# Kernel optimization log

Hardware: AMD Instinct MI355X
Metric: run time of the kernel (lower is better)

The kernel has to match this reference:

```python
import jax, jax.numpy as jnp
import numpy as np

NUM_FEATURES = 256
GROUP_SIZE = 4
NUM_GROUPS = NUM_FEATURES // GROUP_SIZE
EPS = 1e-3


def setup_inputs() -> dict:
    key = jax.random.key(0)
    x = jax.random.normal(key, (64, NUM_FEATURES, 56, 56), dtype=jnp.float32)
    return {"x": x}


def reference(x):
    # Group ZCA whitening (training-mode path of _Whitening.forward).
    b, c, w, h = x.shape
    G, gs = NUM_GROUPS, GROUP_SIZE
    n = b * w * h
    # per-channel mean, grouped: [G, gs, 1]
    m = x.mean(axis=0).reshape(c, -1).mean(axis=-1).reshape(G, gs, 1)
    # [G, gs, b*w*h], mean-centered
    T = x.transpose(1, 0, 2, 3).reshape(G, gs, n) - m
    # unnormalized covariance (matches torch.bmm(T, T^T) in source)
    f_cov = jnp.einsum('gik,gjk->gij', T, T)
    eye = jnp.eye(gs, dtype=x.dtype)
    f_cov_shrinked = (1.0 - EPS) * f_cov + EPS * eye  # [G, gs, gs]
    u, s, _ = jnp.linalg.svd(f_cov_shrinked)
    sqrt_s = jnp.sqrt(s + EPS)[:, :, None]  # [G, gs, 1]
    # pca = u^T T / sqrt(s); zca = u pca
    pca = jnp.einsum('gji,gjk->gik', u, T) / sqrt_s
    zca = jnp.einsum('gij,gjk->gik', u, pca)
    decorrelated = zca.reshape(c, b, w, h).transpose(1, 0, 2, 3)
    return decorrelated
```

## Files before the change

### kernel.cpp

```cpp
#include <hip/hip_runtime.h>
#include <math.h>

#define BATCH   64
#define NFEAT   256
#define GS      4
#define NG      64
#define WH      3136
#define PLANEQ  784
#define NTOT    (BATCH*WH)
#define EPSV    1e-3

typedef float vf4 __attribute__((ext_vector_type(4)));

__global__ __launch_bounds__(256) void wh_reduce(const float* __restrict__ x,
                                                 float* __restrict__ partials) {
    const int blk = blockIdx.x;
    const int b = blk >> 6;
    const int g = blk & 63;
    const vf4* __restrict__ xin =
        (const vf4*)(x + (size_t)b * ((size_t)NFEAT * WH) + (size_t)g * (GS * WH));

    float s0=0.f,s1=0.f,s2=0.f,s3=0.f;
    float p0=0.f,p1=0.f,p2=0.f,p3=0.f,p4=0.f,p5=0.f,p6=0.f,p7=0.f,p8=0.f,p9=0.f;

    for (int q = threadIdx.x; q < PLANEQ; q += 256) {
        vf4 v0 = xin[q];
        vf4 v1 = xin[q + PLANEQ];
        vf4 v2 = xin[q + 2*PLANEQ];
        vf4 v3 = xin[q + 3*PLANEQ];
        #pragma unroll
        for (int k = 0; k < 4; ++k) {
            float a = v0[k], bb = v1[k], c = v2[k], d = v3[k];
            s0 += a; s1 += bb; s2 += c; s3 += d;
            p0 = fmaf(a,  a,  p0);
            p1 = fmaf(a,  bb, p1);
            p2 = fmaf(a,  c,  p2);
            p3 = fmaf(a,  d,  p3);
            p4 = fmaf(bb, bb, p4);
            p5 = fmaf(bb, c,  p5);
            p6 = fmaf(bb, d,  p6);
            p7 = fmaf(c,  c,  p7);
            p8 = fmaf(c,  d,  p8);
            p9 = fmaf(d,  d,  p9);
        }
    }

    float vals[14] = {s0,s1,s2,s3,p0,p1,p2,p3,p4,p5,p6,p7,p8,p9};
    #pragma unroll
    for (int q = 0; q < 14; ++q) {
        float v = vals[q];
        #pragma unroll
        for (int off = 32; off > 0; off >>= 1) v += __shfl_down(v, off, 64);
        vals[q] = v;
    }

    __shared__ float lds[4][14];
    const int wave = threadIdx.x >> 6;
    const int lane = threadIdx.x & 63;
    if (lane == 0) {
        #pragma unroll
        for (int q = 0; q < 14; ++q) lds[wave][q] = vals[q];
    }
    __syncthreads();
    if (threadIdx.x < 14) {
        float v = lds[0][threadIdx.x] + lds[1][threadIdx.x]
                + lds[2][threadIdx.x] + lds[3][threadIdx.x];
        partials[((size_t)(g * BATCH + b)) * 14 + threadIdx.x] = v;
    }
}

__global__ __launch_bounds__(64) void wh_eigen(const float* __restrict__ partials,
                                               float* __restrict__ wm) {
    const int g = blockIdx.x;
    const int b = threadIdx.x;

    const float* base = partials + ((size_t)(g * BATCH + b)) * 14;
    double acc[14];
    #pragma unroll
    for (int q = 0; q < 14; ++q) acc[q] = (double)base[q];

    #pragma unroll
    for (int off = 32; off > 0; off >>= 1) {
        #pragma unroll
        for (int q = 0; q < 14; ++q) acc[q] += __shfl_xor(acc[q], off, 64);
    }

    if (b != 0) return;

    const double n = (double)NTOT;
    double m[4];
    #pragma unroll
    for (int i = 0; i < 4; ++i) m[i] = acc[i] / n;

    const int pi[10] = {0,0,0,0,1,1,1,2,2,3};
    const int pj[10] = {0,1,2,3,1,2,3,2,3,3};

    double A[4][4];
    #pragma unroll
    for (int t = 0; t < 10; ++t) {
        double cov = acc[4 + t] - n * m[pi[t]] * m[pj[t]];
        double v = (1.0 - EPSV) * cov + ((pi[t] == pj[t]) ? EPSV : 0.0);
        A[pi[t]][pj[t]] = v;
        A[pj[t]][pi[t]] = v;
    }

    double V[4][4] = {{1,0,0,0},{0,1,0,0},{0,0,1,0},{0,0,0,1}};

    const double tr = A[0][0] + A[1][1] + A[2][2] + A[3][3];
    const double tol = 1e-26 * tr * tr + 1e-300;

    const int rp[6] = {0,0,0,1,1,2};
    const int rq[6] = {1,2,3,2,3,3};

    for (int sweep = 0; sweep < 10; ++sweep) {
        double off = 0.0;
        #pragma unroll
        for (int t = 0; t < 6; ++t) off += A[rp[t]][rq[t]] * A[rp[t]][rq[t]];
        if (off < tol) break;

        #pragma unroll
        for (int t = 0; t < 6; ++t) {
            const int p = rp[t], q = rq[t];
            double apq = A[p][q];
            if (apq * apq < 1e-60) continue;
            double theta = (A[q][q] - A[p][p]) / (2.0 * apq);
            double tt = ((theta >= 0.0) ? 1.0 : -1.0) /
                        (fabs(theta) + sqrt(theta * theta + 1.0));
            double c = 1.0 / sqrt(tt * tt + 1.0);
            double s = tt * c;
            #pragma unroll
            for (int k = 0; k < 4; ++k) {
                double akp = A[k][p], akq = A[k][q];
                A[k][p] = c * akp - s * akq;
                A[k][q] = s * akp + c * akq;
            }
            #pragma unroll
            for (int k = 0; k < 4; ++k) {
                double apk = A[p][k], aqk = A[q][k];
                A[p][k] = c * apk - s * aqk;
                A[q][k] = s * apk + c * aqk;
            }
            #pragma unroll
            for (int k = 0; k < 4; ++k) {
                double vkp = V[k][p], vkq = V[k][q];
                V[k][p] = c * vkp - s * vkq;
                V[k][q] = s * vkp + c * vkq;
            }
        }
    }

    double isq[4];
    #pragma unroll
    for (int k = 0; k < 4; ++k) isq[k] = 1.0 / sqrt(A[k][k] + EPSV);

    float* wo = wm + g * 20;
    #pragma unroll
    for (int i = 0; i < 4; ++i) {
        #pragma unroll
        for (int j = 0; j < 4; ++j) {
            double w = 0.0;
            #pragma unroll
            for (int k = 0; k < 4; ++k) w += V[i][k] * V[j][k] * isq[k];
            wo[i * 4 + j] = (float)w;
        }
    }
    #pragma unroll
    for (int i = 0; i < 4; ++i) wo[16 + i] = (float)m[i];
}

__global__ __launch_bounds__(256) void wh_apply(const float* __restrict__ x,
                                                const float* __restrict__ wm,
                                                float* __restrict__ out) {
    const int blk = blockIdx.x;
    const int b = blk >> 6;
    const int g = blk & 63;

    __shared__ float sW[20];
    if (threadIdx.x < 20) sW[threadIdx.x] = wm[g * 20 + threadIdx.x];
    __syncthreads();

    float W[4][4], mm[4];
    #pragma unroll
    for (int i = 0; i < 4; ++i) {
        #pragma unroll
        for (int j = 0; j < 4; ++j) W[i][j] = sW[i * 4 + j];
        mm[i] = sW[16 + i];
    }

    const size_t off = (size_t)b * ((size_t)NFEAT * WH) + (size_t)g * (GS * WH);
    const vf4* __restrict__ xin = (const vf4*)(x + off);
    vf4* __restrict__ o = (vf4*)(out + off);

    for (int q = threadIdx.x; q < PLANEQ; q += 256) {
        vf4 v[4];
        v[0] = xin[q];
        v[1] = xin[q + PLANEQ];
        v[2] = xin[q + 2 * PLANEQ];
        v[3] = xin[q + 3 * PLANEQ];

        float c[4][4];
        #pragma unroll
        for (int j = 0; j < 4; ++j) {
            #pragma unroll
            for (int k = 0; k < 4; ++k) c[j][k] = v[j][k] - mm[j];
        }

        #pragma unroll
        for (int i = 0; i < 4; ++i) {
            vf4 r;
            #pragma unroll
            for (int k = 0; k < 4; ++k) {
                r[k] = fmaf(W[i][0], c[0][k],
                       fmaf(W[i][1], c[1][k],
                       fmaf(W[i][2], c[2][k], W[i][3] * c[3][k])));
            }
            __builtin_nontemporal_store(r, &o[q + i * PLANEQ]);
        }
    }
}

extern "C" void kernel_launch(void* const* d_in, const int* in_sizes, int n_in,
                              void* d_out, int out_size, void* d_ws, size_t ws_size,
                              hipStream_t stream) {
    const float* x = (const float*)d_in[0];
    float* out = (float*)d_out;

    float* partials = (float*)d_ws;
    float* wm       = partials + (size_t)NG * BATCH * 14;

    wh_reduce<<<BATCH * NG, 256, 0, stream>>>(x, partials);
    wh_eigen<<<NG, 64, 0, stream>>>(partials, wm);
    wh_apply<<<BATCH * NG, 256, 0, stream>>>(x, wm, out);
}
```

Measured before the change: 110.2 us.

## Fuse eigen solve into reduction via last-block atomic counter; fold mean into bias

```diff
diff --git a/kernel.cpp b/kernel.cpp
--- a/kernel.cpp
+++ b/kernel.cpp
@@ -9,41 +9,54 @@
 #define PLANEQ  784
 #define NTOT    (BATCH*WH)
 #define EPSV    1e-3
+#define PREC    16
 
 typedef float vf4 __attribute__((ext_vector_type(4)));
 
-__global__ __launch_bounds__(256) void wh_reduce(const float* __restrict__ x,
-                                                 float* __restrict__ partials) {
+__global__ __launch_bounds__(256) void wh_reduce_eigen(const float* __restrict__ x,
+                                                       float* __restrict__ partials,
+                                                       float* __restrict__ wm,
+                                                       int* __restrict__ cnt) {
     const int blk = blockIdx.x;
     const int b = blk >> 6;
     const int g = blk & 63;
+    const int tid = threadIdx.x;
     const vf4* __restrict__ xin =
         (const vf4*)(x + (size_t)b * ((size_t)NFEAT * WH) + (size_t)g * (GS * WH));
 
+    vf4 a0 = xin[tid];             vf4 a1 = xin[tid + 256];             vf4 a2 = xin[tid + 512];
+    vf4 b0 = xin[PLANEQ + tid];    vf4 b1 = xin[PLANEQ + tid + 256];    vf4 b2 = xin[PLANEQ + tid + 512];
+    vf4 c0 = xin[2*PLANEQ + tid];  vf4 c1 = xin[2*PLANEQ + tid + 256];  vf4 c2 = xin[2*PLANEQ + tid + 512];
+    vf4 d0 = xin[3*PLANEQ + tid];  vf4 d1 = xin[3*PLANEQ + tid + 256];  vf4 d2 = xin[3*PLANEQ + tid + 512];
+
     float s0=0.f,s1=0.f,s2=0.f,s3=0.f;
     float p0=0.f,p1=0.f,p2=0.f,p3=0.f,p4=0.f,p5=0.f,p6=0.f,p7=0.f,p8=0.f,p9=0.f;
 
-    for (int q = threadIdx.x; q < PLANEQ; q += 256) {
-        vf4 v0 = xin[q];
-        vf4 v1 = xin[q + PLANEQ];
-        vf4 v2 = xin[q + 2*PLANEQ];
-        vf4 v3 = xin[q + 3*PLANEQ];
-        #pragma unroll
-        for (int k = 0; k < 4; ++k) {
-            float a = v0[k], bb = v1[k], c = v2[k], d = v3[k];
-            s0 += a; s1 += bb; s2 += c; s3 += d;
-            p0 = fmaf(a,  a,  p0);
-            p1 = fmaf(a,  bb, p1);
-            p2 = fmaf(a,  c,  p2);
-            p3 = fmaf(a,  d,  p3);
-            p4 = fmaf(bb, bb, p4);
-            p5 = fmaf(bb, c,  p5);
-            p6 = fmaf(bb, d,  p6);
-            p7 = fmaf(c,  c,  p7);
-            p8 = fmaf(c,  d,  p8);
-            p9 = fmaf(d,  d,  p9);
-        }
-    }
+#define ACC4(va, vb, vc, vd)                                         \
+    {                                                                \
+        _Pragma("unroll")                                            \
+        for (int k = 0; k < 4; ++k) {                                \
+            float A = (va)[k], B = (vb)[k], C = (vc)[k], D = (vd)[k];\
+            s0 += A; s1 += B; s2 += C; s3 += D;                      \
+            p0 = fmaf(A, A, p0);  p1 = fmaf(A, B, p1);               \
+            p2 = fmaf(A, C, p2);  p3 = fmaf(A, D, p3);               \
+            p4 = fmaf(B, B, p4);  p5 = fmaf(B, C, p5);               \
+            p6 = fmaf(B, D, p6);  p7 = fmaf(C, C, p7);               \
+            p8 = fmaf(C, D, p8);  p9 = fmaf(D, D, p9);               \
+        }                                                            \
+    }
+
+    ACC4(a0, b0, c0, d0);
+    ACC4(a1, b1, c1, d1);
+    ACC4(a2, b2, c2, d2);
+    if (tid < PLANEQ - 768) {
+        vf4 at = xin[768 + tid];
+        vf4 bt = xin[PLANEQ + 768 + tid];
+        vf4 ct = xin[2*PLANEQ + 768 + tid];
+        vf4 dt = xin[3*PLANEQ + 768 + tid];
+        ACC4(at, bt, ct, dt);
+    }
+#undef ACC4
 
     float vals[14] = {s0,s1,s2,s3,p0,p1,p2,p3,p4,p5,p6,p7,p8,p9};
     #pragma unroll
@@ -55,26 +68,30 @@
     }
 
     __shared__ float lds[4][14];
-    const int wave = threadIdx.x >> 6;
-    const int lane = threadIdx.x & 63;
+    __shared__ int isLast;
+    const int wave = tid >> 6;
+    const int lane = tid & 63;
     if (lane == 0) {
         #pragma unroll
         for (int q = 0; q < 14; ++q) lds[wave][q] = vals[q];
     }
     __syncthreads();
-    if (threadIdx.x < 14) {
-        float v = lds[0][threadIdx.x] + lds[1][threadIdx.x]
-                + lds[2][threadIdx.x] + lds[3][threadIdx.x];
-        partials[((size_t)(g * BATCH + b)) * 14 + threadIdx.x] = v;
-    }
-}
-
-__global__ __launch_bounds__(64) void wh_eigen(const float* __restrict__ partials,
-                                               float* __restrict__ wm) {
-    const int g = blockIdx.x;
-    const int b = threadIdx.x;
-
-    const float* base = partials + ((size_t)(g * BATCH + b)) * 14;
+    if (tid < 14) {
+        float v = lds[0][tid] + lds[1][tid] + lds[2][tid] + lds[3][tid];
+        partials[((size_t)(g * BATCH + b)) * PREC + tid] = v;
+    }
+    __threadfence();
+    __syncthreads();
+    if (tid == 0) {
+        int prev = atomicAdd(&cnt[g], 1);
+        isLast = (prev == BATCH - 1);
+    }
+    __syncthreads();
+    if (!isLast || tid >= 64) return;
+
+    __threadfence();
+
+    const float* base = partials + ((size_t)(g * BATCH + tid)) * PREC;
     double acc[14];
     #pragma unroll
     for (int q = 0; q < 14; ++q) acc[q] = (double)base[q];
@@ -85,7 +102,7 @@
         for (int q = 0; q < 14; ++q) acc[q] += __shfl_xor(acc[q], off, 64);
     }
 
-    if (b != 0) return;
+    if (tid != 0) return;
 
     const double n = (double)NTOT;
     double m[4];
@@ -153,7 +170,8 @@
     #pragma unroll
     for (int k = 0; k < 4; ++k) isq[k] = 1.0 / sqrt(A[k][k] + EPSV);
 
-    float* wo = wm + g * 20;
+    float* wo = wm + g * 24;
+    double Wd[4][4];
     #pragma unroll
     for (int i = 0; i < 4; ++i) {
         #pragma unroll
@@ -161,11 +179,16 @@
             double w = 0.0;
             #pragma unroll
             for (int k = 0; k < 4; ++k) w += V[i][k] * V[j][k] * isq[k];
+            Wd[i][j] = w;
             wo[i * 4 + j] = (float)w;
         }
     }
     #pragma unroll
-    for (int i = 0; i < 4; ++i) wo[16 + i] = (float)m[i];
+    for (int i = 0; i < 4; ++i) {
+        double wmI = Wd[i][0]*m[0] + Wd[i][1]*m[1] + Wd[i][2]*m[2] + Wd[i][3]*m[3];
+        wo[16 + i] = (float)(-wmI);
+        wo[20 + i] = (float)m[i];
+    }
 }
 
 __global__ __launch_bounds__(256) void wh_apply(const float* __restrict__ x,
@@ -174,49 +197,49 @@
     const int blk = blockIdx.x;
     const int b = blk >> 6;
     const int g = blk & 63;
+    const int tid = threadIdx.x;
 
     __shared__ float sW[20];
-    if (threadIdx.x < 20) sW[threadIdx.x] = wm[g * 20 + threadIdx.x];
-    __syncthreads();
-
-    float W[4][4], mm[4];
+    if (tid < 20) sW[tid] = wm[g * 24 + tid];
+    __syncthreads();
+
+    float W[4][4], nwm[4];
     #pragma unroll
     for (int i = 0; i < 4; ++i) {
         #pragma unroll
         for (int j = 0; j < 4; ++j) W[i][j] = sW[i * 4 + j];
-        mm[i] = sW[16 + i];
+        nwm[i] = sW[16 + i];
     }
 
     const size_t off = (size_t)b * ((size_t)NFEAT * WH) + (size_t)g * (GS * WH);
     const vf4* __restrict__ xin = (const vf4*)(x + off);
     vf4* __restrict__ o = (vf4*)(out + off);
 
-    for (int q = threadIdx.x; q < PLANEQ; q += 256) {
-        vf4 v[4];
-        v[0] = xin[q];
-        v[1] = xin[q + PLANEQ];
-        v[2] = xin[q + 2 * PLANEQ];
-        v[3] = xin[q + 3 * PLANEQ];
-
-        float c[4][4];
-        #pragma unroll
-        for (int j = 0; j < 4; ++j) {
-            #pragma unroll
-            for (int k = 0; k < 4; ++k) c[j][k] = v[j][k] - mm[j];
-        }
-
-        #pragma unroll
-        for (int i = 0; i < 4; ++i) {
-            vf4 r;
-            #pragma unroll
-            for (int k = 0; k < 4; ++k) {
-                r[k] = fmaf(W[i][0], c[0][k],
-                       fmaf(W[i][1], c[1][k],
-                       fmaf(W[i][2], c[2][k], W[i][3] * c[3][k])));
-            }
-            __builtin_nontemporal_store(r, &o[q + i * PLANEQ]);
-        }
-    }
+#define APPLY4(q)                                                              \
+    {                                                                          \
+        vf4 v0 = xin[(q)];                                                     \
+        vf4 v1 = xin[(q) + PLANEQ];                                            \
+        vf4 v2 = xin[(q) + 2 * PLANEQ];                                        \
+        vf4 v3 = xin[(q) + 3 * PLANEQ];                                        \
+        _Pragma("unroll")                                                      \
+        for (int i = 0; i < 4; ++i) {                                          \
+            vf4 r;                                                             \
+            _Pragma("unroll")                                                  \
+            for (int k = 0; k < 4; ++k) {                                      \
+                r[k] = fmaf(W[i][0], v0[k],                                    \
+                       fmaf(W[i][1], v1[k],                                    \
+                       fmaf(W[i][2], v2[k],                                    \
+                       fmaf(W[i][3], v3[k], nwm[i]))));                        \
+            }                                                                  \
+            __builtin_nontemporal_store(r, &o[(q) + i * PLANEQ]);              \
+        }                                                                      \
+    }
+
+    APPLY4(tid);
+    APPLY4(tid + 256);
+    APPLY4(tid + 512);
+    if (tid < PLANEQ - 768) APPLY4(tid + 768);
+#undef APPLY4
 }
 
 extern "C" void kernel_launch(void* const* d_in, const int* in_sizes, int n_in,
@@ -226,9 +249,10 @@
     float* out = (float*)d_out;
 
     float* partials = (float*)d_ws;
-    float* wm       = partials + (size_t)NG * BATCH * 14;
-
-    wh_reduce<<<BATCH * NG, 256, 0, stream>>>(x, partials);
-    wh_eigen<<<NG, 64, 0, stream>>>(partials, wm);
+    float* wm       = partials + (size_t)NG * BATCH * PREC;
+    int*   cnt      = (int*)(wm + NG * 24);
+
+    hipMemsetAsync(cnt, 0, NG * sizeof(int), stream);
+    wh_reduce_eigen<<<BATCH * NG, 256, 0, stream>>>(x, partials, wm, cnt);
     wh_apply<<<BATCH * NG, 256, 0, stream>>>(x, wm, out);
 }
```

Measured after the change: 394.9 us. 258% more time.

## Fuse reduce, eigen-solve and apply into one cooperative kernel holding data in registers

Applied to the files above, without the earlier changes.

```diff
diff --git a/kernel.cpp b/kernel.cpp
--- a/kernel.cpp
+++ b/kernel.cpp
@@ -1,5 +1,8 @@
 #include <hip/hip_runtime.h>
+#include <hip/hip_cooperative_groups.h>
 #include <math.h>
+
+namespace cg = cooperative_groups;
 
 #define BATCH   64
 #define NFEAT   256
@@ -9,84 +12,12 @@
 #define PLANEQ  784
 #define NTOT    (BATCH*WH)
 #define EPSV    1e-3
+#define PREC    16
+#define COOP_GRID 2048
 
 typedef float vf4 __attribute__((ext_vector_type(4)));
 
-__global__ __launch_bounds__(256) void wh_reduce(const float* __restrict__ x,
-                                                 float* __restrict__ partials) {
-    const int blk = blockIdx.x;
-    const int b = blk >> 6;
-    const int g = blk & 63;
-    const vf4* __restrict__ xin =
-        (const vf4*)(x + (size_t)b * ((size_t)NFEAT * WH) + (size_t)g * (GS * WH));
-
-    float s0=0.f,s1=0.f,s2=0.f,s3=0.f;
-    float p0=0.f,p1=0.f,p2=0.f,p3=0.f,p4=0.f,p5=0.f,p6=0.f,p7=0.f,p8=0.f,p9=0.f;
-
-    for (int q = threadIdx.x; q < PLANEQ; q += 256) {
-        vf4 v0 = xin[q];
-        vf4 v1 = xin[q + PLANEQ];
-        vf4 v2 = xin[q + 2*PLANEQ];
-        vf4 v3 = xin[q + 3*PLANEQ];
-        #pragma unroll
-        for (int k = 0; k < 4; ++k) {
-            float a = v0[k], bb = v1[k], c = v2[k], d = v3[k];
-            s0 += a; s1 += bb; s2 += c; s3 += d;
-            p0 = fmaf(a,  a,  p0);
-            p1 = fmaf(a,  bb, p1);
-            p2 = fmaf(a,  c,  p2);
-            p3 = fmaf(a,  d,  p3);
-            p4 = fmaf(bb, bb, p4);
-            p5 = fmaf(bb, c,  p5);
-            p6 = fmaf(bb, d,  p6);
-            p7 = fmaf(c,  c,  p7);
-            p8 = fmaf(c,  d,  p8);
-            p9 = fmaf(d,  d,  p9);
-        }
-    }
-
-    float vals[14] = {s0,s1,s2,s3,p0,p1,p2,p3,p4,p5,p6,p7,p8,p9};
-    #pragma unroll
-    for (int q = 0; q < 14; ++q) {
-        float v = vals[q];
-        #pragma unroll
-        for (int off = 32; off > 0; off >>= 1) v += __shfl_down(v, off, 64);
-        vals[q] = v;
-    }
-
-    __shared__ float lds[4][14];
-    const int wave = threadIdx.x >> 6;
-    const int lane = threadIdx.x & 63;
-    if (lane == 0) {
-        #pragma unroll
-        for (int q = 0; q < 14; ++q) lds[wave][q] = vals[q];
-    }
-    __syncthreads();
-    if (threadIdx.x < 14) {
-        float v = lds[0][threadIdx.x] + lds[1][threadIdx.x]
-                + lds[2][threadIdx.x] + lds[3][threadIdx.x];
-        partials[((size_t)(g * BATCH + b)) * 14 + threadIdx.x] = v;
-    }
-}
-
-__global__ __launch_bounds__(64) void wh_eigen(const float* __restrict__ partials,
-                                               float* __restrict__ wm) {
-    const int g = blockIdx.x;
-    const int b = threadIdx.x;
-
-    const float* base = partials + ((size_t)(g * BATCH + b)) * 14;
-    double acc[14];
-    #pragma unroll
-    for (int q = 0; q < 14; ++q) acc[q] = (double)base[q];
-
-    #pragma unroll
-    for (int off = 32; off > 0; off >>= 1) {
-        #pragma unroll
-        for (int q = 0; q < 14; ++q) acc[q] += __shfl_xor(acc[q], off, 64);
-    }
-
-    if (b != 0) return;
-
+__device__ void solve_group(const double* acc, float* wo) {
     const double n = (double)NTOT;
     double m[4];
     #pragma unroll
@@ -105,10 +36,8 @@
     }
 
     double V[4][4] = {{1,0,0,0},{0,1,0,0},{0,0,1,0},{0,0,0,1}};
-
     const double tr = A[0][0] + A[1][1] + A[2][2] + A[3][3];
     const double tol = 1e-26 * tr * tr + 1e-300;
-
     const int rp[6] = {0,0,0,1,1,2};
     const int rq[6] = {1,2,3,2,3,3};
 
@@ -117,7 +46,6 @@
         #pragma unroll
         for (int t = 0; t < 6; ++t) off += A[rp[t]][rq[t]] * A[rp[t]][rq[t]];
         if (off < tol) break;
-
         #pragma unroll
         for (int t = 0; t < 6; ++t) {
             const int p = rp[t], q = rq[t];
@@ -153,7 +81,7 @@
     #pragma unroll
     for (int k = 0; k < 4; ++k) isq[k] = 1.0 / sqrt(A[k][k] + EPSV);
 
-    float* wo = wm + g * 20;
+    double Wd[4][4];
     #pragma unroll
     for (int i = 0; i < 4; ++i) {
         #pragma unroll
@@ -161,11 +89,241 @@
             double w = 0.0;
             #pragma unroll
             for (int k = 0; k < 4; ++k) w += V[i][k] * V[j][k] * isq[k];
+            Wd[i][j] = w;
             wo[i * 4 + j] = (float)w;
         }
     }
     #pragma unroll
-    for (int i = 0; i < 4; ++i) wo[16 + i] = (float)m[i];
+    for (int i = 0; i < 4; ++i) {
+        double wmI = Wd[i][0]*m[0] + Wd[i][1]*m[1] + Wd[i][2]*m[2] + Wd[i][3]*m[3];
+        wo[16 + i] = (float)(-wmI);
+        wo[20 + i] = (float)m[i];
+    }
+}
+
+__global__ __launch_bounds__(256, 8) void wh_fused(const float* __restrict__ x,
+                                                   float* __restrict__ partials,
+                                                   float* __restrict__ wm,
+                                                   float* __restrict__ out) {
+    cg::grid_group grid = cg::this_grid();
+    const int B   = blockIdx.x;
+    const int tid = threadIdx.x;
+    const int b   = B >> 5;
+    const int g0  = (B & 31) << 1;
+
+    const size_t base0 = (size_t)b * ((size_t)NFEAT * WH) + (size_t)g0 * (GS * WH);
+    const vf4* __restrict__ x0 = (const vf4*)(x + base0);
+    const vf4* __restrict__ x1 = x0 + GS * PLANEQ;
+
+    const bool tail = (tid < PLANEQ - 3 * 256);
+    const int  qt   = 768 + (tid & 15);
+
+    vf4 d0[16], d1[16];
+    #pragma unroll
+    for (int c = 0; c < 4; ++c) {
+        #pragma unroll
+        for (int r = 0; r < 3; ++r) {
+            d0[c*4+r] = x0[c*PLANEQ + tid + 256*r];
+            d1[c*4+r] = x1[c*PLANEQ + tid + 256*r];
+        }
+    }
+    #pragma unroll
+    for (int c = 0; c < 4; ++c) {
+        vf4 t0 = x0[c*PLANEQ + qt];
+        vf4 t1 = x1[c*PLANEQ + qt];
+        if (!tail) { t0 = (vf4){0.f,0.f,0.f,0.f}; t1 = (vf4){0.f,0.f,0.f,0.f}; }
+        d0[c*4+3] = t0;
+        d1[c*4+3] = t1;
+    }
+
+    float vv[28];
+    #pragma unroll
+    for (int q = 0; q < 28; ++q) vv[q] = 0.f;
+
+#define REDUCE_TILE(D, OFF)                                              \
+    {                                                                    \
+        _Pragma("unroll")                                                \
+        for (int r = 0; r < 4; ++r) {                                    \
+            _Pragma("unroll")                                            \
+            for (int k = 0; k < 4; ++k) {                                \
+                float A = D[0*4+r][k], Bv = D[1*4+r][k];                 \
+                float C = D[2*4+r][k], Dv = D[3*4+r][k];                 \
+                vv[OFF+0] += A; vv[OFF+1] += Bv;                         \
+                vv[OFF+2] += C; vv[OFF+3] += Dv;                         \
+                vv[OFF+4]  = fmaf(A,  A,  vv[OFF+4]);                    \
+                vv[OFF+5]  = fmaf(A,  Bv, vv[OFF+5]);                    \
+                vv[OFF+6]  = fmaf(A,  C,  vv[OFF+6]);                    \
+                vv[OFF+7]  = fmaf(A,  Dv, vv[OFF+7]);                    \
+                vv[OFF+8]  = fmaf(Bv, Bv, vv[OFF+8]);                    \
+                vv[OFF+9]  = fmaf(Bv, C,  vv[OFF+9]);                    \
+                vv[OFF+10] = fmaf(Bv, Dv, vv[OFF+10]);                   \
+                vv[OFF+11] = fmaf(C,  C,  vv[OFF+11]);                   \
+                vv[OFF+12] = fmaf(C,  Dv, vv[OFF+12]);                   \
+                vv[OFF+13] = fmaf(Dv, Dv, vv[OFF+13]);                   \
+            }                                                            \
+        }                                                                \
+    }
+    REDUCE_TILE(d0, 0);
+    REDUCE_TILE(d1, 14);
+#undef REDUCE_TILE
+
+    #pragma unroll
+    for (int q = 0; q < 28; ++q) {
+        float v = vv[q];
+        #pragma unroll
+        for (int off = 32; off > 0; off >>= 1) v += __shfl_down(v, off, 64);
+        vv[q] = v;
+    }
+
+    __shared__ float lds[4][28];
+    const int wave = tid >> 6;
+    const int lane = tid & 63;
+    if (lane == 0) {
+        #pragma unroll
+        for (int q = 0; q < 28; ++q) lds[wave][q] = vv[q];
+    }
+    __syncthreads();
+    if (tid < 28) {
+        float v = lds[0][tid] + lds[1][tid] + lds[2][tid] + lds[3][tid];
+        const int s = tid / 14, q = tid - s * 14;
+        partials[((size_t)((g0 + s) * BATCH + b)) * PREC + q] = v;
+    }
+
+    grid.sync();
+
+    if (B < NG && tid < 64) {
+        const float* bse = partials + ((size_t)(B * BATCH + tid)) * PREC;
+        double acc[14];
+        #pragma unroll
+        for (int q = 0; q < 14; ++q) acc[q] = (double)bse[q];
+        #pragma unroll
+        for (int off = 32; off > 0; off >>= 1) {
+            #pragma unroll
+            for (int q = 0; q < 14; ++q) acc[q] += __shfl_xor(acc[q], off, 64);
+        }
+        if (tid == 0) solve_group(acc, wm + B * 24);
+    }
+
+    grid.sync();
+
+    __shared__ float sW[40];
+    if (tid < 20)                      sW[tid]        = wm[g0 * 24 + tid];
+    else if (tid >= 32 && tid < 52)    sW[tid - 12]   = wm[(g0 + 1) * 24 + (tid - 32)];
+    __syncthreads();
+
+    float W0[4][4], n0[4], W1[4][4], n1[4];
+    #pragma unroll
+    for (int i = 0; i < 4; ++i) {
+        #pragma unroll
+        for (int j = 0; j < 4; ++j) { W0[i][j] = sW[i*4+j]; W1[i][j] = sW[20+i*4+j]; }
+        n0[i] = sW[16 + i];
+        n1[i] = sW[36 + i];
+    }
+
+    vf4* __restrict__ o0 = (vf4*)(out + base0);
+    vf4* __restrict__ o1 = o0 + GS * PLANEQ;
+
+#define APPLY_TILE(D, W, NW, O)                                          \
+    {                                                                    \
+        _Pragma("unroll")                                                \
+        for (int i = 0; i < 4; ++i) {                                    \
+            _Pragma("unroll")                                            \
+            for (int r = 0; r < 3; ++r) {                                \
+                vf4 rr;                                                  \
+                _Pragma("unroll")                                        \
+                for (int k = 0; k < 4; ++k) {                            \
+                    rr[k] = fmaf(W[i][0], D[0*4+r][k],                   \
+                            fmaf(W[i][1], D[1*4+r][k],                   \
+                            fmaf(W[i][2], D[2*4+r][k],                   \
+                            fmaf(W[i][3], D[3*4+r][k], NW[i]))));        \
+                }                                                        \
+                __builtin_nontemporal_store(rr, &O[i*PLANEQ + tid + 256*r]); \
+            }                                                            \
+            if (tail) {                                                  \
+                vf4 rr;                                                  \
+                _Pragma("unroll")                                        \
+                for (int k = 0; k < 4; ++k) {                            \
+                    rr[k] = fmaf(W[i][0], D[0*4+3][k],                   \
+                            fmaf(W[i][1], D[1*4+3][k],                   \
+                            fmaf(W[i][2], D[2*4+3][k],                   \
+                            fmaf(W[i][3], D[3*4+3][k], NW[i]))));        \
+                }                                                        \
+                __builtin_nontemporal_store(rr, &O[i*PLANEQ + qt]);      \
+            }                                                            \
+        }                                                                \
+    }
+    APPLY_TILE(d0, W0, n0, o0);
+    APPLY_TILE(d1, W1, n1, o1);
+#undef APPLY_TILE
+}
+
+__global__ __launch_bounds__(256) void wh_reduce(const float* __restrict__ x,
+                                                 float* __restrict__ partials) {
+    const int blk = blockIdx.x;
+    const int b = blk >> 6;
+    const int g = blk & 63;
+    const int tid = threadIdx.x;
+    const vf4* __restrict__ xin =
+        (const vf4*)(x + (size_t)b * ((size_t)NFEAT * WH) + (size_t)g * (GS * WH));
+
+    float s0=0.f,s1=0.f,s2=0.f,s3=0.f;
+    float p0=0.f,p1=0.f,p2=0.f,p3=0.f,p4=0.f,p5=0.f,p6=0.f,p7=0.f,p8=0.f,p9=0.f;
+
+    for (int q = tid; q < PLANEQ; q += 256) {
+        vf4 v0 = xin[q];
+        vf4 v1 = xin[q + PLANEQ];
+        vf4 v2 = xin[q + 2*PLANEQ];
+        vf4 v3 = xin[q + 3*PLANEQ];
+        #pragma unroll
+        for (int k = 0; k < 4; ++k) {
+            float A = v0[k], Bv = v1[k], C = v2[k], D = v3[k];
+            s0 += A; s1 += Bv; s2 += C; s3 += D;
+            p0 = fmaf(A, A, p0);   p1 = fmaf(A, Bv, p1);
+            p2 = fmaf(A, C, p2);   p3 = fmaf(A, D, p3);
+            p4 = fmaf(Bv, Bv, p4); p5 = fmaf(Bv, C, p5);
+            p6 = fmaf(Bv, D, p6);  p7 = fmaf(C, C, p7);
+            p8 = fmaf(C, D, p8);   p9 = fmaf(D, D, p9);
+        }
+    }
+
+    float vals[14] = {s0,s1,s2,s3,p0,p1,p2,p3,p4,p5,p6,p7,p8,p9};
+    #pragma unroll
+    for (int q = 0; q < 14; ++q) {
+        float v = vals[q];
+        #pragma unroll
+        for (int off = 32; off > 0; off >>= 1) v += __shfl_down(v, off, 64);
+        vals[q] = v;
+    }
+
+    __shared__ float lds2[4][14];
+    const int wave = tid >> 6;
+    const int lane = tid & 63;
+    if (lane == 0) {
+        #pragma unroll
+        for (int q = 0; q < 14; ++q) lds2[wave][q] = vals[q];
+    }
+    __syncthreads();
+    if (tid < 14) {
+        float v = lds2[0][tid] + lds2[1][tid] + lds2[2][tid] + lds2[3][tid];
+        partials[((size_t)(g * BATCH + b)) * PREC + tid] = v;
+    }
+}
+
+__global__ __launch_bounds__(64) void wh_eigen(const float* __restrict__ partials,
+                                               float* __restrict__ wm) {
+    const int g = blockIdx.x;
+    const int b = threadIdx.x;
+    const float* base = partials + ((size_t)(g * BATCH + b)) * PREC;
+    double acc[14];
+    #pragma unroll
+    for (int q = 0; q < 14; ++q) acc[q] = (double)base[q];
+    #pragma unroll
+    for (int off = 32; off > 0; off >>= 1) {
+        #pragma unroll
+        for (int q = 0; q < 14; ++q) acc[q] += __shfl_xor(acc[q], off, 64);
+    }
+    if (b != 0) return;
+    solve_group(acc, wm + g * 24);
 }
 
 __global__ __launch_bounds__(256) void wh_apply(const float* __restrict__ x,
@@ -174,45 +332,38 @@
     const int blk = blockIdx.x;
     const int b = blk >> 6;
     const int g = blk & 63;
+    const int tid = threadIdx.x;
 
     __shared__ float sW[20];
-    if (threadIdx.x < 20) sW[threadIdx.x] = wm[g * 20 + threadIdx.x];
+    if (tid < 20) sW[tid] = wm[g * 24 + tid];
     __syncthreads();
 
-    float W[4][4], mm[4];
+    float W[4][4], nwm[4];
     #pragma unroll
     for (int i = 0; i < 4; ++i) {
         #pragma unroll
         for (int j = 0; j < 4; ++j) W[i][j] = sW[i * 4 + j];
-        mm[i] = sW[16 + i];
+        nwm[i] = sW[16 + i];
     }
 
     const size_t off = (size_t)b * ((size_t)NFEAT * WH) + (size_t)g * (GS * WH);
     const vf4* __restrict__ xin = (const vf4*)(x + off);
     vf4* __restrict__ o = (vf4*)(out + off);
 
-    for (int q = threadIdx.x; q < PLANEQ; q += 256) {
-        vf4 v[4];
-        v[0] = xin[q];
-        v[1] = xin[q + PLANEQ];
-        v[2] = xin[q + 2 * PLANEQ];
-        v[3] = xin[q + 3 * PLANEQ];
-
-        float c[4][4];
-        #pragma unroll
-        for (int j = 0; j < 4; ++j) {
-            #pragma unroll
-            for (int k = 0; k < 4; ++k) c[j][k] = v[j][k] - mm[j];
-        }
-
+    for (int q = tid; q < PLANEQ; q += 256) {
+        vf4 v0 = xin[q];
+        vf4 v1 = xin[q + PLANEQ];
+        vf4 v2 = xin[q + 2 * PLANEQ];
+        vf4 v3 = xin[q + 3 * PLANEQ];
         #pragma unroll
         for (int i = 0; i < 4; ++i) {
             vf4 r;
             #pragma unroll
             for (int k = 0; k < 4; ++k) {
-                r[k] = fmaf(W[i][0], c[0][k],
-                       fmaf(W[i][1], c[1][k],
-                       fmaf(W[i][2], c[2][k], W[i][3] * c[3][k])));
+                r[k] = fmaf(W[i][0], v0[k],
+                       fmaf(W[i][1], v1[k],
+                       fmaf(W[i][2], v2[k],
+                       fmaf(W[i][3], v3[k], nwm[i]))));
             }
             __builtin_nontemporal_store(r, &o[q + i * PLANEQ]);
         }
@@ -226,7 +377,20 @@
     float* out = (float*)d_out;
 
     float* partials = (float*)d_ws;
-    float* wm       = partials + (size_t)NG * BATCH * 14;
+    float* wm       = partials + (size_t)NG * BATCH * PREC;
+
+    int maxBlk = 0, numCU = 0;
+    hipOccupancyMaxActiveBlocksPerMultiprocessor(&maxBlk, (const void*)wh_fused, 256, 0);
+    hipDeviceGetAttribute(&numCU, hipDeviceAttributeMultiprocessorCount, 0);
+
+    bool coop_ok = (maxBlk * numCU >= COOP_GRID);
+    if (coop_ok) {
+        void* args[4] = {(void*)&x, (void*)&partials, (void*)&wm, (void*)&out};
+        hipError_t e = hipLaunchCooperativeKernel((const void*)wh_fused,
+                                                  dim3(COOP_GRID), dim3(256),
+                                                  args, 0, stream);
+        if (e == hipSuccess) return;
+    }
 
     wh_reduce<<<BATCH * NG, 256, 0, stream>>>(x, partials);
     wh_eigen<<<NG, 64, 0, stream>>>(partials, wm);
```

New measurement: 111.9 us. No clear change (+1.5%).

## Fuse reduce, eigen-solve and apply into one register-resident pass with inter-block flags

Applied to the files above, without the earlier changes.

```diff
diff --git a/kernel.cpp b/kernel.cpp
--- a/kernel.cpp
+++ b/kernel.cpp
@@ -11,82 +11,22 @@
 #define EPSV    1e-3
 
 typedef float vf4 __attribute__((ext_vector_type(4)));
-
-__global__ __launch_bounds__(256) void wh_reduce(const float* __restrict__ x,
-                                                 float* __restrict__ partials) {
-    const int blk = blockIdx.x;
-    const int b = blk >> 6;
-    const int g = blk & 63;
-    const vf4* __restrict__ xin =
-        (const vf4*)(x + (size_t)b * ((size_t)NFEAT * WH) + (size_t)g * (GS * WH));
-
-    float s0=0.f,s1=0.f,s2=0.f,s3=0.f;
-    float p0=0.f,p1=0.f,p2=0.f,p3=0.f,p4=0.f,p5=0.f,p6=0.f,p7=0.f,p8=0.f,p9=0.f;
-
-    for (int q = threadIdx.x; q < PLANEQ; q += 256) {
-        vf4 v0 = xin[q];
-        vf4 v1 = xin[q + PLANEQ];
-        vf4 v2 = xin[q + 2*PLANEQ];
-        vf4 v3 = xin[q + 3*PLANEQ];
-        #pragma unroll
-        for (int k = 0; k < 4; ++k) {
-            float a = v0[k], bb = v1[k], c = v2[k], d = v3[k];
-            s0 += a; s1 += bb; s2 += c; s3 += d;
-            p0 = fmaf(a,  a,  p0);
-            p1 = fmaf(a,  bb, p1);
-            p2 = fmaf(a,  c,  p2);
-            p3 = fmaf(a,  d,  p3);
-            p4 = fmaf(bb, bb, p4);
-            p5 = fmaf(bb, c,  p5);
-            p6 = fmaf(bb, d,  p6);
-            p7 = fmaf(c,  c,  p7);
-            p8 = fmaf(c,  d,  p8);
-            p9 = fmaf(d,  d,  p9);
-        }
-    }
-
-    float vals[14] = {s0,s1,s2,s3,p0,p1,p2,p3,p4,p5,p6,p7,p8,p9};
-    #pragma unroll
-    for (int q = 0; q < 14; ++q) {
-        float v = vals[q];
-        #pragma unroll
-        for (int off = 32; off > 0; off >>= 1) v += __shfl_down(v, off, 64);
-        vals[q] = v;
-    }
-
-    __shared__ float lds[4][14];
-    const int wave = threadIdx.x >> 6;
-    const int lane = threadIdx.x & 63;
-    if (lane == 0) {
-        #pragma unroll
-        for (int q = 0; q < 14; ++q) lds[wave][q] = vals[q];
-    }
-    __syncthreads();
-    if (threadIdx.x < 14) {
-        float v = lds[0][threadIdx.x] + lds[1][threadIdx.x]
-                + lds[2][threadIdx.x] + lds[3][threadIdx.x];
-        partials[((size_t)(g * BATCH + b)) * 14 + threadIdx.x] = v;
-    }
-}
-
-__global__ __launch_bounds__(64) void wh_eigen(const float* __restrict__ partials,
-                                               float* __restrict__ wm) {
-    const int g = blockIdx.x;
-    const int b = threadIdx.x;
-
-    const float* base = partials + ((size_t)(g * BATCH + b)) * 14;
-    double acc[14];
-    #pragma unroll
-    for (int q = 0; q < 14; ++q) acc[q] = (double)base[q];
-
-    #pragma unroll
-    for (int off = 32; off > 0; off >>= 1) {
-        #pragma unroll
-        for (int q = 0; q < 14; ++q) acc[q] += __shfl_xor(acc[q], off, 64);
-    }
-
-    if (b != 0) return;
-
+typedef unsigned long long u64;
+
+#define AL64(p)    __hip_atomic_load((p), __ATOMIC_RELAXED, __HIP_MEMORY_SCOPE_AGENT)
+#define AX64(p,v)  __hip_atomic_exchange((p), (v), __ATOMIC_RELAXED, __HIP_MEMORY_SCOPE_AGENT)
+#define ALI(p)     __hip_atomic_load((p), __ATOMIC_RELAXED, __HIP_MEMORY_SCOPE_AGENT)
+#define AXI(p,v)   __hip_atomic_exchange((p), (v), __ATOMIC_RELAXED, __HIP_MEMORY_SCOPE_AGENT)
+#define AAI(p,v)   __hip_atomic_fetch_add((p), (v), __ATOMIC_RELAXED, __HIP_MEMORY_SCOPE_AGENT)
+
+__device__ inline u64 pack2(float a, float b) {
+    union { float f[2]; u64 u; } t; t.f[0] = a; t.f[1] = b; return t.u;
+}
+__device__ inline void unpack2(u64 u, float& a, float& b) {
+    union { u64 u; float f[2]; } t; t.u = u; a = t.f[0]; b = t.f[1];
+}
+
+__device__ void solve_group(const double* acc, float* wo) {
     const double n = (double)NTOT;
     double m[4];
     #pragma unroll
@@ -105,10 +45,8 @@
     }
 
     double V[4][4] = {{1,0,0,0},{0,1,0,0},{0,0,1,0},{0,0,0,1}};
-
     const double tr = A[0][0] + A[1][1] + A[2][2] + A[3][3];
     const double tol = 1e-26 * tr * tr + 1e-300;
-
     const int rp[6] = {0,0,0,1,1,2};
     const int rq[6] = {1,2,3,2,3,3};
 
@@ -117,7 +55,6 @@
         #pragma unroll
         for (int t = 0; t < 6; ++t) off += A[rp[t]][rq[t]] * A[rp[t]][rq[t]];
         if (off < tol) break;
-
         #pragma unroll
         for (int t = 0; t < 6; ++t) {
             const int p = rp[t], q = rq[t];
@@ -153,7 +90,7 @@
     #pragma unroll
     for (int k = 0; k < 4; ++k) isq[k] = 1.0 / sqrt(A[k][k] + EPSV);
 
-    float* wo = wm + g * 20;
+    double Wd[4][4];
     #pragma unroll
     for (int i = 0; i < 4; ++i) {
         #pragma unroll
@@ -161,60 +98,172 @@
             double w = 0.0;
             #pragma unroll
             for (int k = 0; k < 4; ++k) w += V[i][k] * V[j][k] * isq[k];
+            Wd[i][j] = w;
             wo[i * 4 + j] = (float)w;
         }
     }
     #pragma unroll
-    for (int i = 0; i < 4; ++i) wo[16 + i] = (float)m[i];
-}
-
-__global__ __launch_bounds__(256) void wh_apply(const float* __restrict__ x,
-                                                const float* __restrict__ wm,
-                                                float* __restrict__ out) {
-    const int blk = blockIdx.x;
-    const int b = blk >> 6;
-    const int g = blk & 63;
-
-    __shared__ float sW[20];
-    if (threadIdx.x < 20) sW[threadIdx.x] = wm[g * 20 + threadIdx.x];
-    __syncthreads();
-
-    float W[4][4], mm[4];
-    #pragma unroll
-    for (int i = 0; i < 4; ++i) {
-        #pragma unroll
-        for (int j = 0; j < 4; ++j) W[i][j] = sW[i * 4 + j];
-        mm[i] = sW[16 + i];
-    }
+    for (int i = 0; i < 4; ++i) {
+        double wmI = Wd[i][0]*m[0] + Wd[i][1]*m[1] + Wd[i][2]*m[2] + Wd[i][3]*m[3];
+        wo[16 + i] = (float)(-wmI);
+    }
+}
+
+__global__ __launch_bounds__(256, 2) void wh_onepass(const float* __restrict__ x,
+                                                     u64* __restrict__ partials,
+                                                     u64* __restrict__ wst,
+                                                     int* __restrict__ cnt,
+                                                     int* __restrict__ flag,
+                                                     float* __restrict__ out) {
+    const int g   = blockIdx.x >> 6;
+    const int b   = blockIdx.x & 63;
+    const int tid = threadIdx.x;
 
     const size_t off = (size_t)b * ((size_t)NFEAT * WH) + (size_t)g * (GS * WH);
     const vf4* __restrict__ xin = (const vf4*)(x + off);
+
+    const bool tail = (tid < PLANEQ - 768);
+    const int  qt   = 768 + (tid & 15);
+
+    vf4 d[4][4];
+    #pragma unroll
+    for (int c = 0; c < 4; ++c) {
+        #pragma unroll
+        for (int r = 0; r < 3; ++r) d[c][r] = xin[c * PLANEQ + tid + 256 * r];
+    }
+    #pragma unroll
+    for (int c = 0; c < 4; ++c) {
+        vf4 t = xin[c * PLANEQ + qt];
+        if (!tail) t = (vf4){0.f, 0.f, 0.f, 0.f};
+        d[c][3] = t;
+    }
+
+    float s0=0.f,s1=0.f,s2=0.f,s3=0.f;
+    float p0=0.f,p1=0.f,p2=0.f,p3=0.f,p4=0.f,p5=0.f,p6=0.f,p7=0.f,p8=0.f,p9=0.f;
+    #pragma unroll
+    for (int r = 0; r < 4; ++r) {
+        #pragma unroll
+        for (int k = 0; k < 4; ++k) {
+            float A = d[0][r][k], B = d[1][r][k], C = d[2][r][k], D = d[3][r][k];
+            s0 += A; s1 += B; s2 += C; s3 += D;
+            p0 = fmaf(A, A, p0);  p1 = fmaf(A, B, p1);
+            p2 = fmaf(A, C, p2);  p3 = fmaf(A, D, p3);
+            p4 = fmaf(B, B, p4);  p5 = fmaf(B, C, p5);
+            p6 = fmaf(B, D, p6);  p7 = fmaf(C, C, p7);
+            p8 = fmaf(C, D, p8);  p9 = fmaf(D, D, p9);
+        }
+    }
+
+    float vals[14] = {s0,s1,s2,s3,p0,p1,p2,p3,p4,p5,p6,p7,p8,p9};
+    #pragma unroll
+    for (int q = 0; q < 14; ++q) {
+        float v = vals[q];
+        #pragma unroll
+        for (int o = 32; o > 0; o >>= 1) v += __shfl_down(v, o, 64);
+        vals[q] = v;
+    }
+
+    __shared__ float lds[4][14];
+    __shared__ float sfin[14];
+    __shared__ float sW[20];
+    __shared__ int role;
+    const int wave = tid >> 6;
+    const int lane = tid & 63;
+    if (lane == 0) {
+        #pragma unroll
+        for (int q = 0; q < 14; ++q) lds[wave][q] = vals[q];
+    }
+    __syncthreads();
+    if (tid < 14) sfin[tid] = lds[0][tid] + lds[1][tid] + lds[2][tid] + lds[3][tid];
+    __syncthreads();
+
+    if (tid < 7)
+        AX64(&partials[(size_t)blockIdx.x * 8 + tid], pack2(sfin[2*tid], sfin[2*tid+1]));
+    __syncthreads();
+    if (tid == 0) role = (AAI(&cnt[g], 1) == BATCH - 1) ? 1 : 0;
+    __syncthreads();
+
+    if (role) {
+        double acc[14];
+        if (tid < 64) {
+            u64 r[7];
+            #pragma unroll
+            for (int i = 0; i < 7; ++i)
+                r[i] = AL64(&partials[(size_t)(g * BATCH + tid) * 8 + i]);
+            #pragma unroll
+            for (int i = 0; i < 7; ++i) {
+                float a, bb;
+                unpack2(r[i], a, bb);
+                acc[2*i] = (double)a; acc[2*i+1] = (double)bb;
+            }
+            #pragma unroll
+            for (int o = 32; o > 0; o >>= 1) {
+                #pragma unroll
+                for (int q = 0; q < 14; ++q) acc[q] += __shfl_xor(acc[q], o, 64);
+            }
+        }
+        if (tid == 0) {
+            float wo[20];
+            solve_group(acc, wo);
+            #pragma unroll
+            for (int q = 0; q < 20; ++q) sW[q] = wo[q];
+        }
+        __syncthreads();
+        if (tid < 10)
+            AX64(&wst[(size_t)g * 16 + tid], pack2(sW[2*tid], sW[2*tid+1]));
+        __syncthreads();
+        if (tid == 0) AXI(&flag[g], 1);
+    } else {
+        if (tid == 0) {
+            long long t0 = clock64();
+            while (ALI(&flag[g]) == 0) {
+                if (clock64() - t0 > (1LL << 28)) break;
+                __builtin_amdgcn_s_sleep(8);
+            }
+        }
+        __syncthreads();
+        if (tid < 10) {
+            u64 v = AL64(&wst[(size_t)g * 16 + tid]);
+            float a, bb;
+            unpack2(v, a, bb);
+            sW[2*tid] = a; sW[2*tid+1] = bb;
+        }
+        __syncthreads();
+    }
+
+    float W[4][4], nwm[4];
+    #pragma unroll
+    for (int i = 0; i < 4; ++i) {
+        #pragma unroll
+        for (int j = 0; j < 4; ++j) W[i][j] = sW[i * 4 + j];
+        nwm[i] = sW[16 + i];
+    }
+
     vf4* __restrict__ o = (vf4*)(out + off);
-
-    for (int q = threadIdx.x; q < PLANEQ; q += 256) {
-        vf4 v[4];
-        v[0] = xin[q];
-        v[1] = xin[q + PLANEQ];
-        v[2] = xin[q + 2 * PLANEQ];
-        v[3] = xin[q + 3 * PLANEQ];
-
-        float c[4][4];
-        #pragma unroll
-        for (int j = 0; j < 4; ++j) {
-            #pragma unroll
-            for (int k = 0; k < 4; ++k) c[j][k] = v[j][k] - mm[j];
-        }
-
-        #pragma unroll
-        for (int i = 0; i < 4; ++i) {
-            vf4 r;
-            #pragma unroll
-            for (int k = 0; k < 4; ++k) {
-                r[k] = fmaf(W[i][0], c[0][k],
-                       fmaf(W[i][1], c[1][k],
-                       fmaf(W[i][2], c[2][k], W[i][3] * c[3][k])));
-            }
-            __builtin_nontemporal_store(r, &o[q + i * PLANEQ]);
+    #pragma unroll
+    for (int i = 0; i < 4; ++i) {
+        #pragma unroll
+        for (int r = 0; r < 3; ++r) {
+            vf4 rr;
+            #pragma unroll
+            for (int k = 0; k < 4; ++k) {
+                rr[k] = fmaf(W[i][0], d[0][r][k],
+                        fmaf(W[i][1], d[1][r][k],
+                        fmaf(W[i][2], d[2][r][k],
+                        fmaf(W[i][3], d[3][r][k], nwm[i]))));
+            }
+            __builtin_nontemporal_store(rr, &o[i * PLANEQ + tid + 256 * r]);
+        }
+        if (tail) {
+            vf4 rr;
+            #pragma unroll
+            for (int k = 0; k < 4; ++k) {
+                rr[k] = fmaf(W[i][0], d[0][3][k],
+                        fmaf(W[i][1], d[1][3][k],
+                        fmaf(W[i][2], d[2][3][k],
+                        fmaf(W[i][3], d[3][3][k], nwm[i]))));
+            }
+            __builtin_nontemporal_store(rr, &o[i * PLANEQ + qt]);
         }
     }
 }
@@ -225,10 +274,11 @@
     const float* x = (const float*)d_in[0];
     float* out = (float*)d_out;
 
-    float* partials = (float*)d_ws;
-    float* wm       = partials + (size_t)NG * BATCH * 14;
-
-    wh_reduce<<<BATCH * NG, 256, 0, stream>>>(x, partials);
-    wh_eigen<<<NG, 64, 0, stream>>>(partials, wm);
-    wh_apply<<<BATCH * NG, 256, 0, stream>>>(x, wm, out);
-}
+    u64* partials = (u64*)d_ws;
+    u64* wst      = partials + (size_t)BATCH * NG * 8;
+    int* cnt      = (int*)(wst + (size_t)NG * 16);
+    int* flag     = cnt + NG;
+
+    hipMemsetAsync(cnt, 0, 2 * NG * sizeof(int), stream);
+    wh_onepass<<<BATCH * NG, 256, 0, stream>>>(x, partials, wst, cnt, flag, out);
+}
```

After: 184.5 us. 67.4% more time.
